# Performance work log

Hardware: AMD Instinct MI355X
Metric: run time of the kernel (lower is better)

## Reference

```python
import jax, jax.numpy as jnp
import numpy as np

B, H, W, C = 32, 56, 56, 256
HEADS, WS, SS, MLP = 8, 7, 3, 1024
N = WS * WS
EPS = 1e-6


def _rel_index():
    # matches source: jnp.meshgrid default 'xy' indexing
    coords = jnp.stack(jnp.meshgrid(jnp.arange(WS), jnp.arange(WS)), axis=0)
    cf = coords.reshape(2, -1)
    rc = (cf[:, :, None] - cf[:, None, :]).transpose(1, 2, 0)
    rc = rc + jnp.array([WS - 1, WS - 1])
    rc = rc.at[:, :, 0].multiply(2 * WS - 1)
    return rc.sum(-1)  # (N, N) int


def _attn_mask():
    # standard shifted-window mask: region ids -> -100 where regions differ
    img = np.zeros((H, W), np.float32)
    cnt = 0
    sl = (slice(0, -WS), slice(-WS, -SS), slice(-SS, None))
    for hs in sl:
        for ws_ in sl:
            img[hs, ws_] = cnt
            cnt += 1
    m = jnp.asarray(img).reshape(H // WS, WS, W // WS, WS)
    m = m.transpose(0, 2, 1, 3).reshape(-1, N)  # (nW, N)
    am = m[:, None, :] - m[:, :, None]
    return jnp.where(am != 0, -100.0, 0.0).astype(jnp.float32)  # (nW, N, N)


def _ln(x, scale, bias):
    mu = x.mean(-1, keepdims=True)
    var = ((x - mu) ** 2).mean(-1, keepdims=True)
    return (x - mu) * jax.lax.rsqrt(var + EPS) * scale + bias


def setup_inputs() -> dict:
    key = jax.random.key(0)
    ks = jax.random.split(key, 8)
    s = 0.02
    return {
        "x": jax.random.normal(ks[0], (B, H * W, C), jnp.float32),
        "ln1_scale": jnp.ones((C,), jnp.float32),
        "ln1_bias": jnp.zeros((C,), jnp.float32),
        "qkv_w": jax.random.normal(ks[1], (C, 3 * C), jnp.float32) * s,
        "qkv_b": jnp.zeros((3 * C,), jnp.float32),
        "proj_w": jax.random.normal(ks[2], (C, C), jnp.float32) * s,
        "proj_b": jnp.zeros((C,), jnp.float32),
        "bias_table": jax.random.normal(ks[3], ((2 * WS - 1) ** 2, HEADS), jnp.float32) * s,
        "ln2_scale": jnp.ones((C,), jnp.float32),
        "ln2_bias": jnp.zeros((C,), jnp.float32),
        "fc1_w": jax.random.normal(ks[4], (C, MLP), jnp.float32) * s,
        "fc1_b": jnp.zeros((MLP,), jnp.float32),
        "fc2_w": jax.random.normal(ks[5], (MLP, C), jnp.float32) * s,
        "fc2_b": jnp.zeros((C,), jnp.float32),
    }


def reference(x, ln1_scale, ln1_bias, qkv_w, qkv_b, proj_w, proj_b, bias_table,
              ln2_scale, ln2_bias, fc1_w, fc1_b, fc2_w, fc2_b):
    Bsz, L, Cdim = x.shape
    d = Cdim // HEADS
    scale = d ** (-0.5)
    nW = (H // WS) * (W // WS)

    shortcut = x
    h = _ln(x, ln1_scale, ln1_bias).reshape(Bsz, H, W, Cdim)
    # cyclic shift
    h = jnp.roll(h, (-SS, -SS), axis=(1, 2))
    # window partition -> (Bsz*nW, N, C)
    win = h.reshape(Bsz, H // WS, WS, W // WS, WS, Cdim)
    win = win.transpose(0, 1, 3, 2, 4, 5).reshape(-1, N, Cdim)

    qkv = (win @ qkv_w + qkv_b).reshape(-1, N, 3, HEADS, d).transpose(2, 0, 3, 1, 4)
    q, k, v = qkv[0] * scale, qkv[1], qkv[2]  # (Bw, heads, N, d)
    attn = q @ k.swapaxes(-2, -1)  # (Bw, heads, N, N)

    rpb = bias_table[_rel_index().reshape(-1)].reshape(N, N, HEADS).transpose(2, 0, 1)
    attn = attn + rpb[None]

    mask = _attn_mask()  # (nW, N, N)
    attn = attn.reshape(Bsz, nW, HEADS, N, N) + mask[None, :, None]
    attn = jax.nn.softmax(attn.reshape(-1, HEADS, N, N), axis=-1)

    out = (attn @ v).swapaxes(1, 2).reshape(-1, N, Cdim)
    out = out @ proj_w + proj_b

    # window reverse + reverse shift
    h = out.reshape(Bsz, H // WS, W // WS, WS, WS, Cdim)
    h = h.transpose(0, 1, 3, 2, 4, 5).reshape(Bsz, H, W, Cdim)
    h = jnp.roll(h, (SS, SS), axis=(1, 2)).reshape(Bsz, L, Cdim)

    x = shortcut + h
    y = _ln(x, ln2_scale, ln2_bias)
    y = jax.nn.gelu(y @ fc1_w + fc1_b) @ fc2_w + fc2_b
    return x + y
```

## Files before the change

kernel.cpp:

```cpp
#include <hip/hip_runtime.h>

typedef unsigned short u16;
typedef short short8v __attribute__((ext_vector_type(8)));
typedef float float4v __attribute__((ext_vector_type(4)));

__device__ __forceinline__ float b2f(u16 u) { return __uint_as_float(((unsigned)u) << 16); }
__device__ __forceinline__ u16 f2b(float f) {
    unsigned i = __float_as_uint(f);
    unsigned r = i + 0x7fffu + ((i >> 16) & 1u);
    return (u16)(r >> 16);
}
__device__ __forceinline__ float gelu_f(float x) {
    float z2 = 1.5957691216057308f * (x + 0.044715f * x * x * x);
    float e = __expf(z2);
    return x * (1.0f - 1.0f / (e + 1.0f));
}

typedef const __attribute__((address_space(1))) unsigned int* gas_ptr;
typedef __attribute__((address_space(3))) unsigned int* las_ptr;
__device__ __forceinline__ void gload16(const u16* g, u16* l) {
    __builtin_amdgcn_global_load_lds((gas_ptr)g, (las_ptr)l, 16, 0, 0);
}

__global__ void transpose_k(const float* __restrict__ in, u16* __restrict__ out, int K, int N) {
    int idx = blockIdx.x * 256 + threadIdx.x;
    if (idx < K * N) {
        int n = idx / K;
        int k = idx - n * K;
        out[idx] = f2b(in[(size_t)k * N + n]);
    }
}

__global__ void build_sadd(const float* __restrict__ btab, u16* __restrict__ tbl) {
    int idx = blockIdx.x * 256 + threadIdx.x;
    int key = idx & 63;
    int q = (idx >> 6) & 63;
    int h = (idx >> 12) & 7;
    int type = idx >> 15;
    float v;
    if (key >= 49 || q >= 49) {
        v = -1e30f;
    } else {
        int qy = q / 7, qx = q - qy * 7;
        int ky = key / 7, kx = key - ky * 7;
        int ridx = (qx - kx + 6) * 13 + (qy - ky + 6);
        v = btab[ridx * 8 + h];
        int rcq = (type & 2) ? (qy < 4 ? 1 : 2) : 0;
        int ccq = (type & 1) ? (qx < 4 ? 1 : 2) : 0;
        int rck = (type & 2) ? (ky < 4 ? 1 : 2) : 0;
        int cck = (type & 1) ? (kx < 4 ? 1 : 2) : 0;
        if (rcq * 3 + ccq != rck * 3 + cck) v += -100.0f;
    }
    tbl[idx] = f2b(v);
}

__global__ __launch_bounds__(256) void ln1_win_kernel(
    const float* __restrict__ x, size_t tok0, const float* __restrict__ sc,
    const float* __restrict__ bi, u16* __restrict__ win) {
    int t = blockIdx.x * 4 + (threadIdx.x >> 6);
    int lane = threadIdx.x & 63;
    int wi = t / 49, p = t - wi * 49;
    int b = wi >> 6, w = wi & 63;
    int wr = w >> 3, wc = w & 7;
    int ii = p / 7, jj = p - ii * 7;
    int r = wr * 7 + ii + 3; if (r >= 56) r -= 56;
    int c = wc * 7 + jj + 3; if (c >= 56) c -= 56;
    size_t off = (tok0 + (size_t)(b * 3136 + r * 56 + c)) * 256 + lane * 4;
    float4 d = *(const float4*)(x + off);
    float v0 = d.x, v1 = d.y, v2 = d.z, v3 = d.w;
    float s = v0 + v1 + v2 + v3;
    float ss = v0 * v0 + v1 * v1 + v2 * v2 + v3 * v3;
#pragma unroll
    for (int o = 32; o; o >>= 1) { s += __shfl_xor(s, o, 64); ss += __shfl_xor(ss, o, 64); }
    float mu = s * (1.0f / 256.0f);
    float rs = rsqrtf(ss * (1.0f / 256.0f) - mu * mu + 1e-6f);
    float4 s4 = *(const float4*)(sc + lane * 4);
    float4 b4 = *(const float4*)(bi + lane * 4);
    ushort4 o4;
    o4.x = f2b((v0 - mu) * rs * s4.x + b4.x);
    o4.y = f2b((v1 - mu) * rs * s4.y + b4.y);
    o4.z = f2b((v2 - mu) * rs * s4.z + b4.z);
    o4.w = f2b((v3 - mu) * rs * s4.w + b4.w);
    *(ushort4*)(win + (size_t)t * 256 + lane * 4) = o4;
}

template <int EPI>
__global__ __launch_bounds__(256) void gemm_bt(
    const u16* __restrict__ A, const u16* __restrict__ Bt, const float* __restrict__ bias,
    const u16* __restrict__ res, void* __restrict__ Cout, int M, int N, int K) {
    __shared__ __align__(16) u16 smem[17408];
    u16* As = smem;
    u16* Bs = smem + 8192;
    int tid = threadIdx.x;
    int m0 = blockIdx.y * 128, n0 = blockIdx.x * 128;
    int lane = tid & 63, wave = tid >> 6;
    int wm = (wave >> 1) * 64, wn = (wave & 1) * 64;
    int lrow = lane & 15, qd = lane >> 4;
    int c0 = wave << 2;
    int rsub0 = lane >> 3;
    int kc = (((lane & 7) ^ rsub0) << 3);
    float4v acc[4][4] = {};
    int kTiles = K >> 6;
    for (int kt = 0; kt < kTiles; ++kt) {
        int k0 = kt << 6;
#pragma unroll
        for (int i = 0; i < 4; ++i) {
            int c = c0 + i;
            int rsub = (c << 3) + rsub0;
            int rA = m0 + rsub; if (rA >= M) rA = M - 1;
            gload16(A + (size_t)rA * K + k0 + kc, As + (c << 9));
            gload16(Bt + (size_t)(n0 + rsub) * K + k0 + kc, Bs + (c << 9));
        }
        __syncthreads();
#pragma unroll
        for (int ks = 0; ks < 64; ks += 32) {
            short8v af[4], bfr[4];
#pragma unroll
            for (int mi = 0; mi < 4; ++mi) {
                int row = wm + mi * 16 + lrow;
                int s = ((ks >> 3) + qd) ^ (row & 7);
                af[mi] = *(const short8v*)&As[row * 64 + (s << 3)];
            }
#pragma unroll
            for (int ni = 0; ni < 4; ++ni) {
                int row = wn + ni * 16 + lrow;
                int s = ((ks >> 3) + qd) ^ (row & 7);
                bfr[ni] = *(const short8v*)&Bs[row * 64 + (s << 3)];
            }
#pragma unroll
            for (int mi = 0; mi < 4; ++mi)
#pragma unroll
                for (int ni = 0; ni < 4; ++ni)
                    acc[mi][ni] = __builtin_amdgcn_mfma_f32_16x16x32_bf16(
                        af[mi], bfr[ni], acc[mi][ni], 0, 0, 0);
        }
        __syncthreads();
    }
    if (EPI == 2) {
#pragma unroll
        for (int ni = 0; ni < 4; ++ni) {
            int col = n0 + wn + ni * 16 + lrow;
            float bv = bias[col];
#pragma unroll
            for (int mi = 0; mi < 4; ++mi) {
#pragma unroll
                for (int rr = 0; rr < 4; ++rr) {
                    int row = m0 + wm + mi * 16 + qd * 4 + rr;
                    if (row < M) {
                        float v = acc[mi][ni][rr] + bv + b2f(res[(size_t)row * N + col]);
                        ((float*)Cout)[(size_t)row * N + col] = v;
                    }
                }
            }
        }
    } else {
#pragma unroll
        for (int ni = 0; ni < 4; ++ni) {
            float bv = bias[n0 + wn + ni * 16 + lrow];
#pragma unroll
            for (int mi = 0; mi < 4; ++mi) {
#pragma unroll
                for (int rr = 0; rr < 4; ++rr) {
                    float v = acc[mi][ni][rr] + bv;
                    if (EPI == 1) v = gelu_f(v);
                    smem[(wm + mi * 16 + qd * 4 + rr) * 136 + wn + ni * 16 + lrow] = f2b(v);
                }
            }
        }
        __syncthreads();
        u16* outp = (u16*)Cout;
#pragma unroll
        for (int j = 0; j < 8; ++j) {
            int slot = j * 256 + tid;
            int row = slot >> 4, cs = (slot & 15) << 3;
            short8v vv = *(const short8v*)&smem[row * 136 + cs];
            int grow = m0 + row;
            if (grow < M)
                *(short8v*)(outp + (size_t)grow * N + n0 + cs) = vv;
        }
    }
}

__global__ __launch_bounds__(256) void attn_kernel(
    const u16* __restrict__ qkv, const u16* __restrict__ sadd, u16* __restrict__ attno) {
    __shared__ __align__(16) u16 lds[4][6272];
    int wave = threadIdx.x >> 6, lane = threadIdx.x & 63;
    u16* Plds = lds[wave];
    u16* Vt = lds[wave] + 4096;
    float* sums = (float*)(lds[wave] + 6144);
    int u = blockIdx.x * 4 + wave;
    int wi = u >> 3, h = u & 7;
    int w = wi & 63;
    int type = (((w >> 3) == 7) ? 2 : 0) | (((w & 7) == 7) ? 1 : 0);
    const u16* base = qkv + (size_t)wi * 49 * 768 + h * 32;
    int lrow = lane & 15, qd = lane >> 4;

#pragma unroll
    for (int z = 0; z < 4; ++z)
        *(short8v*)&Vt[(z * 64 + lane) * 8] = (short8v){0, 0, 0, 0, 0, 0, 0, 0};
    for (int idx = lane; idx < 196; idx += 64) {
        int t = idx >> 2, part = (idx & 3) << 3;
        uint4 vd = *(const uint4*)(base + 512 + (size_t)t * 768 + part);
        const u16* vs = (const u16*)&vd;
#pragma unroll
        for (int e = 0; e < 8; ++e) {
            int c = part + e;
            Vt[c * 64 + ((((t >> 3) ^ (c & 7)) << 3) | (t & 7))] = vs[e];
        }
    }

    short8v qf[4], kf[4];
#pragma unroll
    for (int i = 0; i < 4; ++i) {
        qf[i] = *(const short8v*)(base + (size_t)(16 * i + lrow) * 768 + qd * 8);
        kf[i] = *(const short8v*)(base + 256 + (size_t)(16 * i + lrow) * 768 + qd * 8);
    }
    float4v s[4][4];
#pragma unroll
    for (int i = 0; i < 4; ++i)
#pragma unroll
        for (int j = 0; j < 4; ++j)
            s[i][j] = __builtin_amdgcn_mfma_f32_16x16x32_bf16(
                qf[i], kf[j], (float4v){0.f, 0.f, 0.f, 0.f}, 0, 0, 0);

    const float scale = 0.17677669529663687f;
    const u16* tb = sadd + ((size_t)(type * 8 + h) << 12);
#pragma unroll
    for (int i = 0; i < 4; ++i)
#pragma unroll
        for (int j = 0; j < 4; ++j)
#pragma unroll
            for (int rr = 0; rr < 4; ++rr) {
                int q = 16 * i + qd * 4 + rr, key = 16 * j + lrow;
                float v = s[i][j][rr] * scale + b2f(tb[q * 64 + key]);
                if (j == 3 && lrow > 0) v = -1e30f;
                s[i][j][rr] = v;
            }
    float rmx[4][4];
#pragma unroll
    for (int i = 0; i < 4; ++i)
#pragma unroll
        for (int rr = 0; rr < 4; ++rr) {
            float m = fmaxf(fmaxf(s[i][0][rr], s[i][1][rr]), fmaxf(s[i][2][rr], s[i][3][rr]));
#pragma unroll
            for (int o = 1; o < 16; o <<= 1) m = fmaxf(m, __shfl_xor(m, o, 64));
            rmx[i][rr] = m;
        }
    int hi = lrow >> 3, lo = lrow & 7;
#pragma unroll
    for (int i = 0; i < 4; ++i)
#pragma unroll
        for (int rr = 0; rr < 4; ++rr) {
            int q = 16 * i + qd * 4 + rr;
            float e0 = __expf(s[i][0][rr] - rmx[i][rr]);
            float e1 = __expf(s[i][1][rr] - rmx[i][rr]);
            float e2 = __expf(s[i][2][rr] - rmx[i][rr]);
            float e3 = __expf(s[i][3][rr] - rmx[i][rr]);
            float sm = (e0 + e1) + (e2 + e3);
#pragma unroll
            for (int o = 1; o < 16; o <<= 1) sm += __shfl_xor(sm, o, 64);
            int q64 = q * 64, q7 = q & 7;
            Plds[q64 + ((((0 + hi) ^ q7) << 3) | lo)] = f2b(e0);
            Plds[q64 + ((((2 + hi) ^ q7) << 3) | lo)] = f2b(e1);
            Plds[q64 + ((((4 + hi) ^ q7) << 3) | lo)] = f2b(e2);
            Plds[q64 + ((((6 + hi) ^ q7) << 3) | lo)] = f2b(e3);
            if (lrow == 0) sums[q] = sm;
        }

    float4v o[2][4] = {};
#pragma unroll
    for (int ks = 0; ks < 2; ++ks) {
        short8v av[2], bp[4];
#pragma unroll
        for (int ci = 0; ci < 2; ++ci) {
            int c = 16 * ci + lrow;
            av[ci] = *(const short8v*)&Vt[c * 64 + ((((ks << 2) + qd) ^ (c & 7)) << 3)];
        }
#pragma unroll
        for (int qj = 0; qj < 4; ++qj) {
            int q = 16 * qj + lrow;
            bp[qj] = *(const short8v*)&Plds[q * 64 + ((((ks << 2) + qd) ^ (q & 7)) << 3)];
        }
#pragma unroll
        for (int ci = 0; ci < 2; ++ci)
#pragma unroll
            for (int qj = 0; qj < 4; ++qj)
                o[ci][qj] = __builtin_amdgcn_mfma_f32_16x16x32_bf16(
                    av[ci], bp[qj], o[ci][qj], 0, 0, 0);
    }
#pragma unroll
    for (int qj = 0; qj < 4; ++qj) {
        int q = 16 * qj + lrow;
        if (q < 49) {
            float inv = 1.0f / sums[q];
            u16* op = attno + ((size_t)wi * 49 + q) * 256 + h * 32;
#pragma unroll
            for (int ci = 0; ci < 2; ++ci) {
                ushort4 d4;
                d4.x = f2b(o[ci][qj][0] * inv);
                d4.y = f2b(o[ci][qj][1] * inv);
                d4.z = f2b(o[ci][qj][2] * inv);
                d4.w = f2b(o[ci][qj][3] * inv);
                *(ushort4*)(op + 16 * ci + qd * 4) = d4;
            }
        }
    }
}

__global__ __launch_bounds__(256) void scatter_ln2_kernel(
    const float* __restrict__ x, size_t tok0, const u16* __restrict__ projo,
    const float* __restrict__ sc, const float* __restrict__ bi,
    u16* __restrict__ x2, u16* __restrict__ ln2o) {
    int tk = blockIdx.x * 4 + (threadIdx.x >> 6);
    int lane = threadIdx.x & 63;
    int b = tk / 3136, l = tk - b * 3136;
    int r = l / 56, c = l - r * 56;
    int r2 = r + 53; if (r2 >= 56) r2 -= 56;
    int c2 = c + 53; if (c2 >= 56) c2 -= 56;
    int wr = r2 / 7, ri = r2 - wr * 7;
    int wc = c2 / 7, ci = c2 - wc * 7;
    size_t t = ((size_t)(b * 64 + wr * 8 + wc)) * 49 + ri * 7 + ci;
    size_t loff = (size_t)tk * 256 + lane * 4;
    size_t goff = (tok0 + tk) * 256 + lane * 4;
    float4 xd = *(const float4*)(x + goff);
    ushort4 pd = *(const ushort4*)(projo + t * 256 + lane * 4);
    float v0 = xd.x + b2f(pd.x);
    float v1 = xd.y + b2f(pd.y);
    float v2 = xd.z + b2f(pd.z);
    float v3 = xd.w + b2f(pd.w);
    ushort4 o4;
    o4.x = f2b(v0); o4.y = f2b(v1); o4.z = f2b(v2); o4.w = f2b(v3);
    *(ushort4*)(x2 + loff) = o4;
    float s = v0 + v1 + v2 + v3;
    float ss = v0 * v0 + v1 * v1 + v2 * v2 + v3 * v3;
#pragma unroll
    for (int o = 32; o; o >>= 1) { s += __shfl_xor(s, o, 64); ss += __shfl_xor(ss, o, 64); }
    float mu = s * (1.0f / 256.0f);
    float rs = rsqrtf(ss * (1.0f / 256.0f) - mu * mu + 1e-6f);
    float4 s4 = *(const float4*)(sc + lane * 4);
    float4 b4 = *(const float4*)(bi + lane * 4);
    ushort4 n4;
    n4.x = f2b((v0 - mu) * rs * s4.x + b4.x);
    n4.y = f2b((v1 - mu) * rs * s4.y + b4.y);
    n4.z = f2b((v2 - mu) * rs * s4.z + b4.z);
    n4.w = f2b((v3 - mu) * rs * s4.w + b4.w);
    *(ushort4*)(ln2o + loff) = n4;
}

extern "C" void kernel_launch(void* const* d_in, const int* in_sizes, int n_in,
                              void* d_out, int out_size, void* d_ws, size_t ws_size,
                              hipStream_t stream) {
    const float* x     = (const float*)d_in[0];
    const float* ln1s  = (const float*)d_in[1];
    const float* ln1b  = (const float*)d_in[2];
    const float* qkvw  = (const float*)d_in[3];
    const float* qkvb  = (const float*)d_in[4];
    const float* projw = (const float*)d_in[5];
    const float* projb = (const float*)d_in[6];
    const float* btab  = (const float*)d_in[7];
    const float* ln2s  = (const float*)d_in[8];
    const float* ln2b  = (const float*)d_in[9];
    const float* fc1w  = (const float*)d_in[10];
    const float* fc1b  = (const float*)d_in[11];
    const float* fc2w  = (const float*)d_in[12];
    const float* fc2b  = (const float*)d_in[13];
    float* out = (float*)d_out;
    char* ws = (char*)d_ws;

    u16* wt_qkv  = (u16*)(ws + 0);
    u16* wt_proj = (u16*)(ws + 393216);
    u16* wt_fc1  = (u16*)(ws + 524288);
    u16* wt_fc2  = (u16*)(ws + 1048576);
    u16* saddt   = (u16*)(ws + 1572864);
    const size_t base = 1835008;

    build_sadd<<<512, 256, 0, stream>>>(btab, saddt);
    transpose_k<<<768, 256, 0, stream>>>(qkvw, wt_qkv, 256, 768);
    transpose_k<<<256, 256, 0, stream>>>(projw, wt_proj, 256, 256);
    transpose_k<<<1024, 256, 0, stream>>>(fc1w, wt_fc1, 256, 1024);
    transpose_k<<<1024, 256, 0, stream>>>(fc2w, wt_fc2, 1024, 256);

    int NB = 16;
    while (NB > 1 && base + (size_t)NB * 3136 * 3072 > ws_size) NB >>= 1;
    const size_t T = (size_t)NB * 3136;

    u16* regA = (u16*)(ws + base);
    u16* regB = (u16*)(ws + base + T * 512);
    u16* regX = (u16*)(ws + base + T * 512 + T * 2048);

    for (int c0 = 0; c0 < 32; c0 += NB) {
        size_t tok0 = (size_t)c0 * 3136;
        float* outc = out + tok0 * 256;
        int Mc = (int)T;
        int gx = (Mc + 127) / 128;

        ln1_win_kernel<<<Mc / 4, 256, 0, stream>>>(x, tok0, ln1s, ln1b, regA);
        gemm_bt<0><<<dim3(6, gx), 256, 0, stream>>>(regA, wt_qkv, qkvb, nullptr,
                                                    regB, Mc, 768, 256);
        attn_kernel<<<NB * 128, 256, 0, stream>>>(regB, saddt, regA);
        gemm_bt<0><<<dim3(2, gx), 256, 0, stream>>>(regA, wt_proj, projb, nullptr,
                                                    regB, Mc, 256, 256);
        scatter_ln2_kernel<<<Mc / 4, 256, 0, stream>>>(x, tok0, regB, ln2s, ln2b,
                                                       regX, regA);
        gemm_bt<1><<<dim3(8, gx), 256, 0, stream>>>(regA, wt_fc1, fc1b, nullptr,
                                                    regB, Mc, 1024, 256);
        gemm_bt<2><<<dim3(2, gx), 256, 0, stream>>>(regB, wt_fc2, fc2b, regX,
                                                    outc, Mc, 256, 1024);
    }
}
```

Before: 802.3 us.

## Double-buffer GEMM LDS tiles to overlap global loads with MFMA

```diff
diff --git a/kernel.cpp b/kernel.cpp
--- a/kernel.cpp
+++ b/kernel.cpp
@@ -88,9 +88,7 @@
 __global__ __launch_bounds__(256) void gemm_bt(
     const u16* __restrict__ A, const u16* __restrict__ Bt, const float* __restrict__ bias,
     const u16* __restrict__ res, void* __restrict__ Cout, int M, int N, int K) {
-    __shared__ __align__(16) u16 smem[17408];
-    u16* As = smem;
-    u16* Bs = smem + 8192;
+    __shared__ __align__(16) u16 smem[2][16384];
     int tid = threadIdx.x;
     int m0 = blockIdx.y * 128, n0 = blockIdx.x * 128;
     int lane = tid & 63, wave = tid >> 6;
@@ -101,17 +99,37 @@
     int kc = (((lane & 7) ^ rsub0) << 3);
     float4v acc[4][4] = {};
     int kTiles = K >> 6;
+
+    const u16* Aps[4];
+    const u16* Bps[4];
+#pragma unroll
+    for (int i = 0; i < 4; ++i) {
+        int c = c0 + i;
+        int rsub = (c << 3) + rsub0;
+        int rA = m0 + rsub; if (rA >= M) rA = M - 1;
+        Aps[i] = A + (size_t)rA * K + kc;
+        Bps[i] = Bt + (size_t)(n0 + rsub) * K + kc;
+    }
+#pragma unroll
+    for (int i = 0; i < 4; ++i) {
+        gload16(Aps[i], &smem[0][(c0 + i) << 9]);
+        gload16(Bps[i], &smem[0][8192 + ((c0 + i) << 9)]);
+    }
+    asm volatile("s_waitcnt vmcnt(0)" ::: "memory");
+    __builtin_amdgcn_s_barrier();
+
     for (int kt = 0; kt < kTiles; ++kt) {
-        int k0 = kt << 6;
-#pragma unroll
-        for (int i = 0; i < 4; ++i) {
-            int c = c0 + i;
-            int rsub = (c << 3) + rsub0;
-            int rA = m0 + rsub; if (rA >= M) rA = M - 1;
-            gload16(A + (size_t)rA * K + k0 + kc, As + (c << 9));
-            gload16(Bt + (size_t)(n0 + rsub) * K + k0 + kc, Bs + (c << 9));
-        }
-        __syncthreads();
+        int cur = kt & 1;
+        if (kt + 1 < kTiles) {
+            int k0 = (kt + 1) << 6;
+#pragma unroll
+            for (int i = 0; i < 4; ++i) {
+                gload16(Aps[i] + k0, &smem[cur ^ 1][(c0 + i) << 9]);
+                gload16(Bps[i] + k0, &smem[cur ^ 1][8192 + ((c0 + i) << 9)]);
+            }
+        }
+        const u16* As = smem[cur];
+        const u16* Bs = smem[cur] + 8192;
 #pragma unroll
         for (int ks = 0; ks < 64; ks += 32) {
             short8v af[4], bfr[4];
@@ -134,7 +152,8 @@
                     acc[mi][ni] = __builtin_amdgcn_mfma_f32_16x16x32_bf16(
                         af[mi], bfr[ni], acc[mi][ni], 0, 0, 0);
         }
-        __syncthreads();
+        asm volatile("s_waitcnt vmcnt(0)" ::: "memory");
+        __builtin_amdgcn_s_barrier();
     }
     if (EPI == 2) {
 #pragma unroll
@@ -154,6 +173,7 @@
             }
         }
     } else {
+        u16* ep = (u16*)smem;
 #pragma unroll
         for (int ni = 0; ni < 4; ++ni) {
             float bv = bias[n0 + wn + ni * 16 + lrow];
@@ -163,7 +183,7 @@
                 for (int rr = 0; rr < 4; ++rr) {
                     float v = acc[mi][ni][rr] + bv;
                     if (EPI == 1) v = gelu_f(v);
-                    smem[(wm + mi * 16 + qd * 4 + rr) * 136 + wn + ni * 16 + lrow] = f2b(v);
+                    ep[(wm + mi * 16 + qd * 4 + rr) * 136 + wn + ni * 16 + lrow] = f2b(v);
                 }
             }
         }
@@ -173,7 +193,7 @@
         for (int j = 0; j < 8; ++j) {
             int slot = j * 256 + tid;
             int row = slot >> 4, cs = (slot & 15) << 3;
-            short8v vv = *(const short8v*)&smem[row * 136 + cs];
+            short8v vv = *(const short8v*)&ep[row * 136 + cs];
             int grow = m0 + row;
             if (grow < M)
                 *(short8v*)(outp + (size_t)grow * N + n0 + cs) = vv;
```

Result: faster. 761.8 us (-5.1%).
